# Optimization experiments

Measured on AMD Instinct MI355X. Metric: run time of the kernel, lower is better.

The kernel has to match this reference:

```python
import jax, jax.numpy as jnp
import numpy as np
from jax import lax

B, C, H, W = 8, 64, 96, 96
OC = 64
KH = KW = 3
DG = 1
STRIDE = 1
PAD = 1
DIL = 1


def setup_inputs() -> dict:
    key = jax.random.key(0)
    k1, k2, k3, k4, k5 = jax.random.split(key, 5)
    x = jax.random.normal(k1, (B, C, H, W), jnp.float32)
    off_ch = DG * 3 * KH * KW
    # small random offset/mask conv params (the original inits them to zero,
    # which would make offsets degenerate; small values exercise the sampler)
    w_off = jax.random.normal(k2, (off_ch, C, KH, KW), jnp.float32) * 0.01
    b_off = jax.random.normal(k3, (off_ch,), jnp.float32) * 0.01
    stdv = 1.0 / float(np.sqrt(C * KH * KW))
    weight = jax.random.uniform(k4, (OC, C, KH, KW), jnp.float32, -stdv, stdv)
    bias = jax.random.uniform(k5, (OC,), jnp.float32, -stdv, stdv)
    return {"x": x, "w_off": w_off, "b_off": b_off, "weight": weight, "bias": bias}


def _deform_conv(x, w_off, b_off, weight, bias):
    Bt, Ct, Ht, Wt = x.shape
    K = KH * KW
    # standard conv producing offsets + mask logits
    om = lax.conv_general_dilated(
        x, w_off, (STRIDE, STRIDE), ((PAD, PAD), (PAD, PAD)),
        rhs_dilation=(DIL, DIL), dimension_numbers=("NCHW", "OIHW", "NCHW"),
    ) + b_off[None, :, None, None]
    o1, o2, m = jnp.split(om, 3, axis=1)  # each [B, DG*K, Ho, Wo]
    Ho, Wo = o1.shape[2], o1.shape[3]
    mask = jax.nn.sigmoid(m).reshape(Bt, DG, 1, K, Ho, Wo)
    off_y = o1.reshape(Bt, DG, K, Ho, Wo)
    off_x = o2.reshape(Bt, DG, K, Ho, Wo)
    # base sampling grid: p = out_pos*stride - pad + k*dilation + offset
    kk = jnp.arange(K)
    base_y = (kk // KW)[:, None] * DIL + (jnp.arange(Ho) * STRIDE - PAD)[None, :]  # [K, Ho]
    base_x = (kk % KW)[:, None] * DIL + (jnp.arange(Wo) * STRIDE - PAD)[None, :]   # [K, Wo]
    py = off_y + base_y[None, None, :, :, None].astype(x.dtype)  # [B, DG, K, Ho, Wo]
    px = off_x + base_x[None, None, :, None, :].astype(x.dtype)
    y0 = jnp.floor(py)
    x0 = jnp.floor(px)
    ly = py - y0
    lx = px - x0
    Cg = Ct // DG
    xg = x.reshape(Bt, DG, Cg, Ht * Wt)

    def gath(xf, idx):  # xf [Cg, H*W], idx [K*Ho*Wo]
        return jnp.take(xf, idx, axis=1)

    gather = jax.vmap(jax.vmap(gath))  # over B, DG

    sampled = jnp.zeros((Bt, DG, Cg, K, Ho, Wo), x.dtype)
    for dy, dx, wgt in ((0, 0, (1 - ly) * (1 - lx)), (0, 1, (1 - ly) * lx),
                        (1, 0, ly * (1 - lx)), (1, 1, ly * lx)):
        yy = y0 + dy
        xx = x0 + dx
        valid = (yy >= 0) & (yy < Ht) & (xx >= 0) & (xx < Wt)
        yi = jnp.clip(yy, 0, Ht - 1).astype(jnp.int32)
        xi = jnp.clip(xx, 0, Wt - 1).astype(jnp.int32)
        idx = (yi * Wt + xi).reshape(Bt, DG, K * Ho * Wo)
        v = gather(xg, idx).reshape(Bt, DG, Cg, K, Ho, Wo)
        sampled = sampled + v * (wgt * valid)[:, :, None]
    sampled = sampled * mask  # modulated
    wr = weight.reshape(OC, DG, Cg, K)
    out = jnp.einsum("bgckhw,ogck->bohw", sampled, wr) + bias[None, :, None, None]
    return out


def reference(x, w_off, b_off, weight, bias):
    return _deform_conv(x, w_off, b_off, weight, bias)
```

## Files before the change

### kernel.cpp

```cpp
#include <hip/hip_runtime.h>
#include <math.h>

#define Bn 8
#define Cn 64
#define Hn 96
#define Wn 96
#define HWn (Hn*Wn)
#define OCn 64
#define Kn 9
#define OFFCn 27
#define NPIX (Bn*HWn)
#define PGRPS (NPIX/64)

#define WPK1_N 15552
#define WPK2_N 36864
#define WS_DWORDS (45*NPIX + WPK1_N + WPK2_N)
#define WS_BYTES  ((size_t)WS_DWORDS*4)

__global__ __launch_bounds__(256) void dcn_wprep(
    const float* __restrict__ w_off,
    const float* __restrict__ weight,
    float* __restrict__ wpk1,
    float* __restrict__ wpk2)
{
    const int g = blockIdx.x * 256 + threadIdx.x;
    if (g < WPK1_N) {
        const int c_all = g / 243;
        const int och   = (g % 243) / 9;
        const int ki    = g % 9;
        wpk1[g] = w_off[(och * 64 + c_all) * 9 + ki];
    }
    const int h = g - WPK1_N;
    if (h >= 0 && h < WPK2_N) {
        const int ki  = h % 9;
        const int j   = (h / 9) % 8;
        const int c16 = (h / 72) % 16;
        const int ch  = (h / 1152) % 4;
        const int wv  = h / 4608;
        const int oc  = wv * 8 + j;
        const int c   = ch * 16 + c16;
        wpk2[h] = weight[(oc * 64 + c) * 9 + ki];
    }
}

__global__ __launch_bounds__(256, 2) void dcn_k1(
    const float* __restrict__ x,
    const float* __restrict__ wpk1,
    const float* __restrict__ b_off,
    float* __restrict__ pwbuf,
    int*   __restrict__ abuf)
{
    __shared__ float lds[4 * 64 * OFFCn];

    const int tid  = threadIdx.x;
    const int lane = tid & 63;
    const int wv   = tid >> 6;
    const int cbase = __builtin_amdgcn_readfirstlane(wv * 16);

    const int p  = blockIdx.x * 64 + lane;
    const int b  = p / HWn;
    const int hw = p % HWn;
    const int ho = hw / Wn;
    const int wo = hw % Wn;

    const float* xb = x + b * (Cn * HWn);

    int   toff[Kn];
    float tval[Kn];
#pragma unroll
    for (int ki = 0; ki < Kn; ++ki) {
        const int yy = ho + ki / 3 - 1, xx = wo + ki % 3 - 1;
        const bool v = (yy >= 0) && (yy < Hn) && (xx >= 0) && (xx < Wn);
        toff[ki] = min(max(yy, 0), Hn - 1) * Wn + min(max(xx, 0), Wn - 1);
        tval[ki] = v ? 1.0f : 0.0f;
    }

    float om[OFFCn];
#pragma unroll
    for (int j = 0; j < OFFCn; ++j) om[j] = 0.0f;

    const float* wstream = wpk1 + cbase * 243;
    for (int ci = 0; ci < 16; ++ci) {
        const float* xc = xb + (cbase + ci) * HWn;
        float xk[Kn];
#pragma unroll
        for (int ki = 0; ki < Kn; ++ki)
            xk[ki] = xc[toff[ki]] * tval[ki];

        const float* wc = wstream + ci * 243;
#pragma unroll
        for (int och = 0; och < OFFCn; ++och) {
            const float* wp = wc + och * 9;
            float a = om[och];
#pragma unroll
            for (int ki = 0; ki < Kn; ++ki)
                a = fmaf(xk[ki], wp[ki], a);
            om[och] = a;
        }
    }

#pragma unroll
    for (int j = 0; j < OFFCn; ++j)
        lds[(wv * 64 + lane) * OFFCn + j] = om[j];
    __syncthreads();
#pragma unroll
    for (int j = 0; j < OFFCn; ++j) {
        float a = b_off[j];
#pragma unroll
        for (int ww = 0; ww < 4; ++ww)
            a += lds[(ww * 64 + lane) * OFFCn + j];
        om[j] = a;
    }

    float pw0[Kn], pw1[Kn], pw2[Kn], pw3[Kn];
    int   pav[Kn];
#pragma unroll
    for (int ki = 0; ki < Kn; ++ki) {
        const float py = om[ki]      + (float)(ki / 3 + ho - 1);
        const float px = om[Kn + ki] + (float)(ki % 3 + wo - 1);
        const float m  = 1.0f / (1.0f + __expf(-om[2 * Kn + ki]));

        const float y0f = floorf(py), x0f = floorf(px);
        const float ly = py - y0f, lx = px - x0f;
        const int iy0 = (int)y0f, ix0 = (int)x0f;
        const int iy1 = iy0 + 1,  ix1 = ix0 + 1;

        const float vy0 = (iy0 >= 0 && iy0 < Hn) ? 1.0f : 0.0f;
        const float vy1 = (iy1 >= 0 && iy1 < Hn) ? 1.0f : 0.0f;
        const float vx0 = (ix0 >= 0 && ix0 < Wn) ? 1.0f : 0.0f;
        const float vx1 = (ix1 >= 0 && ix1 < Wn) ? 1.0f : 0.0f;

        const int iy0c = min(max(iy0, 0), Hn - 1);
        const int iy1c = min(max(iy1, 0), Hn - 1);
        const int ix0c = min(max(ix0, 0), Wn - 1);
        const int ix1c = min(max(ix1, 0), Wn - 1);

        pw0[ki] = m * (1.0f - ly) * (1.0f - lx) * vy0 * vx0;
        pw1[ki] = m * (1.0f - ly) * lx          * vy0 * vx1;
        pw2[ki] = m * ly          * (1.0f - lx) * vy1 * vx0;
        pw3[ki] = m * ly          * lx          * vy1 * vx1;
        const int pa  = iy0c * Wn + ix0c;
        const int dx  = ix1c - ix0c;
        const int dyw = (iy1c - iy0c) * Wn;
        pav[ki] = pa | (dx << 16) | (dyw << 17);
    }

    if (wv == 0) {
#pragma unroll
        for (int ki = 0; ki < Kn; ++ki) pwbuf[(0 * Kn + ki) * NPIX + p] = pw0[ki];
#pragma unroll
        for (int ki = 0; ki < Kn; ++ki) abuf[ki * NPIX + p] = pav[ki];
    } else if (wv == 1) {
#pragma unroll
        for (int ki = 0; ki < Kn; ++ki) pwbuf[(1 * Kn + ki) * NPIX + p] = pw1[ki];
    } else if (wv == 2) {
#pragma unroll
        for (int ki = 0; ki < Kn; ++ki) pwbuf[(2 * Kn + ki) * NPIX + p] = pw2[ki];
    } else {
#pragma unroll
        for (int ki = 0; ki < Kn; ++ki) pwbuf[(3 * Kn + ki) * NPIX + p] = pw3[ki];
    }
}

__global__ __launch_bounds__(512, 4) void dcn_k2(
    const float* __restrict__ x,
    const float* __restrict__ wpk2,
    const float* __restrict__ bias,
    const float* __restrict__ pwbuf,
    const int*   __restrict__ abuf,
    float* __restrict__ out)
{
    __shared__ float smp[16 * Kn * 64];

    const int tid  = threadIdx.x;
    const int lane = tid & 63;
    const int wv   = tid >> 6;
    const int ocb  = __builtin_amdgcn_readfirstlane(wv * 8);

    const int p  = blockIdx.x * 64 + lane;
    const int b  = p / HWn;
    const int hw = p % HWn;

    const float* xb = x + b * (Cn * HWn);

    float pw0[Kn], pw1[Kn], pw2[Kn], pw3[Kn];
    int   pav[Kn];
#pragma unroll
    for (int ki = 0; ki < Kn; ++ki) pw0[ki] = pwbuf[(0 * Kn + ki) * NPIX + p];
#pragma unroll
    for (int ki = 0; ki < Kn; ++ki) pw1[ki] = pwbuf[(1 * Kn + ki) * NPIX + p];
#pragma unroll
    for (int ki = 0; ki < Kn; ++ki) pw2[ki] = pwbuf[(2 * Kn + ki) * NPIX + p];
#pragma unroll
    for (int ki = 0; ki < Kn; ++ki) pw3[ki] = pwbuf[(3 * Kn + ki) * NPIX + p];
#pragma unroll
    for (int ki = 0; ki < Kn; ++ki) pav[ki] = abuf[ki * NPIX + p];

    float acc[8];
#pragma unroll
    for (int j = 0; j < 8; ++j) acc[j] = bias[ocb + j];

    const float* wbase = wpk2 + __builtin_amdgcn_readfirstlane(wv * 4 * 1152);

    for (int ch = 0; ch < 4; ++ch) {
#pragma unroll
        for (int cc = 0; cc < 2; ++cc) {
            const int cin = (wv << 1) | cc;
            const float* xc = xb + (ch * 16 + cin) * HWn;
#pragma unroll
            for (int ki = 0; ki < Kn; ++ki) {
                const int av  = pav[ki];
                const int pa  = av & 0xFFFF;
                const int dx  = (av >> 16) & 1;
                const int dyw = av >> 17;
                const float* bp = xc + pa;
                const float v00 = bp[0];
                const float v01 = bp[dx];
                const float v10 = bp[dyw];
                const float v11 = bp[dyw + dx];
                smp[(cin * Kn + ki) * 64 + lane] =
                    pw0[ki] * v00 + pw1[ki] * v01 + pw2[ki] * v10 + pw3[ki] * v11;
            }
        }
        __syncthreads();

        const float* ws2 = wbase + ch * 1152;
#pragma unroll 2
        for (int c16 = 0; c16 < 16; ++c16) {
            float sv[Kn];
#pragma unroll
            for (int ki = 0; ki < Kn; ++ki)
                sv[ki] = smp[(c16 * Kn + ki) * 64 + lane];
            const float* wc = ws2 + c16 * 72;
#pragma unroll
            for (int j = 0; j < 8; ++j) {
                const float* wp = wc + j * 9;
                float a = acc[j];
#pragma unroll
                for (int ki = 0; ki < Kn; ++ki)
                    a = fmaf(sv[ki], wp[ki], a);
                acc[j] = a;
            }
        }
        __syncthreads();
    }

    float* ob = out + b * (OCn * HWn) + hw;
#pragma unroll
    for (int j = 0; j < 8; ++j)
        ob[(ocb + j) * HWn] = acc[j];
}

__global__ __launch_bounds__(64) void dcn_r1(
    const float* __restrict__ x,
    const float* __restrict__ w_off,
    const float* __restrict__ b_off,
    const float* __restrict__ weight,
    const float* __restrict__ bias,
    float* __restrict__ out)
{
    const int p  = blockIdx.x * 64 + threadIdx.x;
    const int b  = p / HWn;
    const int hw = p % HWn;
    const int ho = hw / Wn;
    const int wo = hw % Wn;
    const float* xb = x + b * (Cn * HWn);

    float om[OFFCn];
#pragma unroll
    for (int j = 0; j < OFFCn; ++j) om[j] = b_off[j];

    int   toff[Kn];
    float tval[Kn];
#pragma unroll
    for (int ki = 0; ki < Kn; ++ki) {
        const int yy = ho + ki / 3 - 1, xx = wo + ki % 3 - 1;
        const bool v = (yy >= 0) && (yy < Hn) && (xx >= 0) && (xx < Wn);
        toff[ki] = min(max(yy, 0), Hn - 1) * Wn + min(max(xx, 0), Wn - 1);
        tval[ki] = v ? 1.0f : 0.0f;
    }
    for (int c = 0; c < Cn; ++c) {
        const float* xc = xb + c * HWn;
        float xk[Kn];
#pragma unroll
        for (int ki = 0; ki < Kn; ++ki) xk[ki] = xc[toff[ki]] * tval[ki];
        const float* wc = w_off + c * Kn;
#pragma unroll
        for (int och = 0; och < OFFCn; ++och) {
            const float* wp = wc + och * (Cn * Kn);
            float a = om[och];
#pragma unroll
            for (int ki = 0; ki < Kn; ++ki) a = fmaf(xk[ki], wp[ki], a);
            om[och] = a;
        }
    }
    float pw0[Kn], pw1[Kn], pw2[Kn], pw3[Kn];
    int   pa[Kn], pdx[Kn], pdyw[Kn];
#pragma unroll
    for (int ki = 0; ki < Kn; ++ki) {
        const float py = om[ki]      + (float)(ki / 3 + ho - 1);
        const float px = om[Kn + ki] + (float)(ki % 3 + wo - 1);
        const float m  = 1.0f / (1.0f + __expf(-om[2 * Kn + ki]));
        const float y0f = floorf(py), x0f = floorf(px);
        const float ly = py - y0f, lx = px - x0f;
        const int iy0 = (int)y0f, ix0 = (int)x0f;
        const int iy1 = iy0 + 1,  ix1 = ix0 + 1;
        const float vy0 = (iy0 >= 0 && iy0 < Hn) ? 1.0f : 0.0f;
        const float vy1 = (iy1 >= 0 && iy1 < Hn) ? 1.0f : 0.0f;
        const float vx0 = (ix0 >= 0 && ix0 < Wn) ? 1.0f : 0.0f;
        const float vx1 = (ix1 >= 0 && ix1 < Wn) ? 1.0f : 0.0f;
        const int iy0c = min(max(iy0, 0), Hn - 1);
        const int iy1c = min(max(iy1, 0), Hn - 1);
        const int ix0c = min(max(ix0, 0), Wn - 1);
        const int ix1c = min(max(ix1, 0), Wn - 1);
        pw0[ki] = m * (1.0f - ly) * (1.0f - lx) * vy0 * vx0;
        pw1[ki] = m * (1.0f - ly) * lx          * vy0 * vx1;
        pw2[ki] = m * ly          * (1.0f - lx) * vy1 * vx0;
        pw3[ki] = m * ly          * lx          * vy1 * vx1;
        pa[ki]   = iy0c * Wn + ix0c;
        pdx[ki]  = ix1c - ix0c;
        pdyw[ki] = (iy1c - iy0c) * Wn;
    }
    float acc[OCn];
#pragma unroll
    for (int oc = 0; oc < OCn; ++oc) acc[oc] = bias[oc];
    for (int c = 0; c < Cn; ++c) {
        const float* xc = xb + c * HWn;
        float s[Kn];
#pragma unroll
        for (int ki = 0; ki < Kn; ++ki) {
            const float* bp = xc + pa[ki];
            s[ki] = pw0[ki] * bp[0] + pw1[ki] * bp[pdx[ki]]
                  + pw2[ki] * bp[pdyw[ki]] + pw3[ki] * bp[pdyw[ki] + pdx[ki]];
        }
        const float* wc = weight + c * Kn;
#pragma unroll
        for (int oc = 0; oc < OCn; ++oc) {
            const float* wp = wc + oc * (Cn * Kn);
            float a = acc[oc];
#pragma unroll
            for (int ki = 0; ki < Kn; ++ki) a = fmaf(s[ki], wp[ki], a);
            acc[oc] = a;
        }
    }
    float* ob = out + b * (OCn * HWn) + hw;
#pragma unroll
    for (int oc = 0; oc < OCn; ++oc) ob[oc * HWn] = acc[oc];
}

extern "C" void kernel_launch(void* const* d_in, const int* in_sizes, int n_in,
                              void* d_out, int out_size, void* d_ws, size_t ws_size,
                              hipStream_t stream) {
    const float* x      = (const float*)d_in[0];
    const float* w_off  = (const float*)d_in[1];
    const float* b_off  = (const float*)d_in[2];
    const float* weight = (const float*)d_in[3];
    const float* bias   = (const float*)d_in[4];
    float* out = (float*)d_out;

    if (ws_size >= WS_BYTES) {
        float* pwbuf = (float*)d_ws;
        int*   abuf  = (int*)((float*)d_ws + 36 * NPIX);
        float* wpk1  = (float*)d_ws + 45 * NPIX;
        float* wpk2  = wpk1 + WPK1_N;
        hipLaunchKernelGGL(dcn_wprep, dim3((WPK1_N + WPK2_N + 255) / 256), dim3(256),
                           0, stream, w_off, weight, wpk1, wpk2);
        hipLaunchKernelGGL(dcn_k1, dim3(PGRPS), dim3(256), 0, stream,
                           x, wpk1, b_off, pwbuf, abuf);
        hipLaunchKernelGGL(dcn_k2, dim3(PGRPS), dim3(512), 0, stream,
                           x, wpk2, bias, pwbuf, abuf, out);
    } else {
        hipLaunchKernelGGL(dcn_r1, dim3(NPIX / 64), dim3(64), 0, stream,
                           x, w_off, b_off, weight, bias, out);
    }
}
```

Measured before the change: 256.7 us.

## Move deformable-conv output GEMM onto bf16 MFMA with hi/lo split

Replaces the scalar FMA contraction in the second kernel with 16x16x32 bf16 MFMA instructions. The bilinear samples are split into high and low bf16 parts so that activation precision is roughly preserved, while the weights are pre-packed into bf16 MFMA fragment layout. The block shrinks from 512 to 256 threads and the channel loop becomes 8 chunks of 8 channels staged through LDS. This aims to cut the VALU-bound GEMM cost, at the price of rounding the weights to bf16, which loses precision, and adds extra work to pack the samples.

Measured after the change: 261.5 us. About the same (+1.8%).

```diff
diff --git a/kernel.cpp b/kernel.cpp
--- a/kernel.cpp
+++ b/kernel.cpp
@@ -13,15 +13,26 @@
 #define PGRPS (NPIX/64)
 
 #define WPK1_N 15552
-#define WPK2_N 36864
-#define WS_DWORDS (45*NPIX + WPK1_N + WPK2_N)
+#define WPK2M_SHORTS 131072
+#define WS_DWORDS (45*NPIX + WPK1_N + WPK2M_SHORTS/2)
 #define WS_BYTES  ((size_t)WS_DWORDS*4)
+
+typedef __attribute__((ext_vector_type(8))) short short8v;
+typedef __attribute__((ext_vector_type(4))) float f32x4;
+
+static __device__ __forceinline__ unsigned short bf16_rne(float f) {
+    unsigned int u = __float_as_uint(f);
+    return (unsigned short)((u + 0x7FFFu + ((u >> 16) & 1u)) >> 16);
+}
+static __device__ __forceinline__ float bf16_back(unsigned short h) {
+    return __uint_as_float(((unsigned int)h) << 16);
+}
 
 __global__ __launch_bounds__(256) void dcn_wprep(
     const float* __restrict__ w_off,
     const float* __restrict__ weight,
     float* __restrict__ wpk1,
-    float* __restrict__ wpk2)
+    short* __restrict__ wpk2m)
 {
     const int g = blockIdx.x * 256 + threadIdx.x;
     if (g < WPK1_N) {
@@ -30,16 +41,22 @@
         const int ki    = g % 9;
         wpk1[g] = w_off[(och * 64 + c_all) * 9 + ki];
     }
-    const int h = g - WPK1_N;
-    if (h >= 0 && h < WPK2_N) {
-        const int ki  = h % 9;
-        const int j   = (h / 9) % 8;
-        const int c16 = (h / 72) % 16;
-        const int ch  = (h / 1152) % 4;
-        const int wv  = h / 4608;
-        const int oc  = wv * 8 + j;
-        const int c   = ch * 16 + c16;
-        wpk2[h] = weight[(oc * 64 + c) * 9 + ki];
+    if (g < WPK2M_SHORTS / 8) {
+        const int lane = g & 63;
+        const int oct  = (g >> 6) & 3;
+        const int c    = g >> 8;
+        const int oc   = oct * 16 + (lane & 15);
+        const float* wsrc = weight + (oc * 64 + c) * 9;
+        short8v v;
+#pragma unroll
+        for (int j = 0; j < 8; ++j) {
+            const int s = ((lane >> 4) & 3) * 8 + j;
+            float f = 0.0f;
+            if (s <= 8)                f = wsrc[s];
+            else if (s >= 16 && s <= 24) f = wsrc[s - 16];
+            v[j] = (short)bf16_rne(f);
+        }
+        ((short8v*)wpk2m)[g] = v;
     }
 }
 
@@ -162,24 +179,24 @@
     }
 }
 
-__global__ __launch_bounds__(512, 4) void dcn_k2(
+__global__ __launch_bounds__(256, 2) void dcn_k2(
     const float* __restrict__ x,
-    const float* __restrict__ wpk2,
+    const short* __restrict__ wpk2m,
     const float* __restrict__ bias,
     const float* __restrict__ pwbuf,
     const int*   __restrict__ abuf,
     float* __restrict__ out)
 {
-    __shared__ float smp[16 * Kn * 64];
+    __shared__ short smp[32 * 64 * 8];
 
     const int tid  = threadIdx.x;
     const int lane = tid & 63;
     const int wv   = tid >> 6;
-    const int ocb  = __builtin_amdgcn_readfirstlane(wv * 8);
-
-    const int p  = blockIdx.x * 64 + lane;
-    const int b  = p / HWn;
-    const int hw = p % HWn;
+
+    const int p0  = blockIdx.x * 64;
+    const int b   = p0 / HWn;
+    const int hwb = p0 % HWn;
+    const int p   = p0 + lane;
 
     const float* xb = x + b * (Cn * HWn);
 
@@ -196,17 +213,18 @@
 #pragma unroll
     for (int ki = 0; ki < Kn; ++ki) pav[ki] = abuf[ki * NPIX + p];
 
-    float acc[8];
-#pragma unroll
-    for (int j = 0; j < 8; ++j) acc[j] = bias[ocb + j];
-
-    const float* wbase = wpk2 + __builtin_amdgcn_readfirstlane(wv * 4 * 1152);
-
-    for (int ch = 0; ch < 4; ++ch) {
+    f32x4 acc[4];
+#pragma unroll
+    for (int oct = 0; oct < 4; ++oct) acc[oct] = (f32x4){0.f, 0.f, 0.f, 0.f};
+
+    const short8v* afrags = (const short8v*)wpk2m;
+
+    for (int chunk = 0; chunk < 8; ++chunk) {
 #pragma unroll
         for (int cc = 0; cc < 2; ++cc) {
-            const int cin = (wv << 1) | cc;
-            const float* xc = xb + (ch * 16 + cin) * HWn;
+            const int cl = (wv << 1) | cc;
+            const float* xc = xb + (chunk * 8 + cl) * HWn;
+            unsigned short hi[Kn], lo[Kn];
 #pragma unroll
             for (int ki = 0; ki < Kn; ++ki) {
                 const int av  = pav[ki];
@@ -214,41 +232,49 @@
                 const int dx  = (av >> 16) & 1;
                 const int dyw = av >> 17;
                 const float* bp = xc + pa;
-                const float v00 = bp[0];
-                const float v01 = bp[dx];
-                const float v10 = bp[dyw];
-                const float v11 = bp[dyw + dx];
-                smp[(cin * Kn + ki) * 64 + lane] =
-                    pw0[ki] * v00 + pw1[ki] * v01 + pw2[ki] * v10 + pw3[ki] * v11;
+                const float v = pw0[ki] * bp[0] + pw1[ki] * bp[dx]
+                              + pw2[ki] * bp[dyw] + pw3[ki] * bp[dyw + dx];
+                hi[ki] = bf16_rne(v);
+                lo[ki] = bf16_rne(v - bf16_back(hi[ki]));
             }
+            short8v h0, h1, l0, l1;
+#pragma unroll
+            for (int j = 0; j < 8; ++j) { h0[j] = (short)hi[j]; l0[j] = (short)lo[j]; }
+            h1 = (short8v){(short)hi[8], 0, 0, 0, 0, 0, 0, 0};
+            l1 = (short8v){(short)lo[8], 0, 0, 0, 0, 0, 0, 0};
+            const int r0 = cl * 4;
+            *(short8v*)&smp[((r0 + 0) * 64 + lane) * 8] = h0;
+            *(short8v*)&smp[((r0 + 1) * 64 + lane) * 8] = h1;
+            *(short8v*)&smp[((r0 + 2) * 64 + lane) * 8] = l0;
+            *(short8v*)&smp[((r0 + 3) * 64 + lane) * 8] = l1;
         }
         __syncthreads();
 
-        const float* ws2 = wbase + ch * 1152;
-#pragma unroll 2
-        for (int c16 = 0; c16 < 16; ++c16) {
-            float sv[Kn];
-#pragma unroll
-            for (int ki = 0; ki < Kn; ++ki)
-                sv[ki] = smp[(c16 * Kn + ki) * 64 + lane];
-            const float* wc = ws2 + c16 * 72;
-#pragma unroll
-            for (int j = 0; j < 8; ++j) {
-                const float* wp = wc + j * 9;
-                float a = acc[j];
-#pragma unroll
-                for (int ki = 0; ki < Kn; ++ki)
-                    a = fmaf(sv[ki], wp[ki], a);
-                acc[j] = a;
+#pragma unroll
+        for (int ks = 0; ks < 8; ++ks) {
+            const short8v bfrag = *(const short8v*)
+                &smp[((ks * 4 + (lane >> 4)) * 64 + wv * 16 + (lane & 15)) * 8];
+#pragma unroll
+            for (int oct = 0; oct < 4; ++oct) {
+                const short8v afrag =
+                    afrags[(((chunk * 8 + ks) * 4) + oct) * 64 + lane];
+                acc[oct] = __builtin_amdgcn_mfma_f32_16x16x32_bf16(
+                    afrag, bfrag, acc[oct], 0, 0, 0);
             }
         }
         __syncthreads();
     }
 
-    float* ob = out + b * (OCn * HWn) + hw;
-#pragma unroll
-    for (int j = 0; j < 8; ++j)
-        ob[(ocb + j) * HWn] = acc[j];
+    const int pxl = wv * 16 + (lane & 15);
+    float* ob = out + b * (OCn * HWn) + hwb + pxl;
+#pragma unroll
+    for (int oct = 0; oct < 4; ++oct) {
+#pragma unroll
+        for (int r = 0; r < 4; ++r) {
+            const int oc = oct * 16 + ((lane >> 4) & 3) * 4 + r;
+            ob[oc * HWn] = acc[oct][r] + bias[oc];
+        }
+    }
 }
 
 __global__ __launch_bounds__(64) void dcn_r1(
@@ -362,13 +388,13 @@
         float* pwbuf = (float*)d_ws;
         int*   abuf  = (int*)((float*)d_ws + 36 * NPIX);
         float* wpk1  = (float*)d_ws + 45 * NPIX;
-        float* wpk2  = wpk1 + WPK1_N;
-        hipLaunchKernelGGL(dcn_wprep, dim3((WPK1_N + WPK2_N + 255) / 256), dim3(256),
-                           0, stream, w_off, weight, wpk1, wpk2);
+        short* wpk2m = (short*)(wpk1 + WPK1_N);
+        hipLaunchKernelGGL(dcn_wprep, dim3(64), dim3(256), 0, stream,
+                           w_off, weight, wpk1, wpk2m);
         hipLaunchKernelGGL(dcn_k1, dim3(PGRPS), dim3(256), 0, stream,
                            x, wpk1, b_off, pwbuf, abuf);
-        hipLaunchKernelGGL(dcn_k2, dim3(PGRPS), dim3(512), 0, stream,
-                           x, wpk2, bias, pwbuf, abuf, out);
+        hipLaunchKernelGGL(dcn_k2, dim3(PGRPS), dim3(256), 0, stream,
+                           x, wpk2m, bias, pwbuf, abuf, out);
     } else {
         hipLaunchKernelGGL(dcn_r1, dim3(NPIX / 64), dim3(64), 0, stream,
                            x, w_off, b_off, weight, bias, out);
```
